# Kernel optimization log

Hardware: AMD Instinct MI355X
Metric: run time of the kernel (lower is better)

Reference implementation:

```python
import jax, jax.numpy as jnp
import numpy as np

EPS = 1e-5


def setup_inputs() -> dict:
    key = jax.random.key(0)
    ks = jax.random.split(key, 4)
    N, E, D, L = 100000, 1600000, 128, 3
    x = jax.random.normal(ks[0], (N, D), dtype=jnp.float32)
    edge_index = jax.random.randint(ks[1], (2, E), 0, N, dtype=jnp.int64)
    # torch Linear weight layout [out, in]; kaiming-ish scale
    W = jax.random.normal(ks[2], (L, D, D), dtype=jnp.float32) / np.sqrt(D)
    b = jnp.zeros((L, D), dtype=jnp.float32)
    gamma = jnp.ones((L, D), dtype=jnp.float32)
    beta = jnp.zeros((L, D), dtype=jnp.float32)
    return {"x": x, "edge_index": edge_index, "W": W, "b": b,
            "gamma": gamma, "beta": beta}


def reference(x, edge_index, W, b, gamma, beta):
    N = x.shape[0]
    L = W.shape[0]
    # add_self_loops
    loops = jnp.arange(N, dtype=edge_index.dtype)
    ei = jnp.concatenate([edge_index, jnp.stack([loops, loops])], axis=1)
    row, col = ei[0], ei[1]  # source, target (PyG source_to_target flow)
    # degree of target nodes (includes self loops)
    deg = jax.ops.segment_sum(jnp.ones(col.shape, x.dtype), col, num_segments=N)
    deg_inv_sqrt = jnp.where(deg > 0, deg ** -0.5, jnp.array(0.0, x.dtype))
    norm = deg_inv_sqrt[row] * deg_inv_sqrt[col]  # [E+N]
    for l in range(L):
        h = x @ W[l].T  # Linear, no bias
        # gather source messages, scale, scatter-add to targets
        out = jax.ops.segment_sum(norm[:, None] * h[row], col, num_segments=N)
        out = out + b[l]
        # NodeNorm 'm': subtract per-node (row) mean over features
        out = out - jnp.mean(out, axis=1, keepdims=True)
        # BatchNorm1d (training mode: biased batch stats over node axis)
        mu = jnp.mean(out, axis=0)
        var = jnp.var(out, axis=0)
        x = gamma[l] * (out - mu) * jax.lax.rsqrt(var + EPS) + beta[l]
    return x
```

## Files before the change

kernel.cpp:

```cpp
#include <hip/hip_runtime.h>

#define D 128
#define EPSV 1e-5f

typedef _Float16 f16;
typedef __attribute__((ext_vector_type(8))) _Float16 f16x8;
typedef __attribute__((ext_vector_type(4))) _Float16 f16x4;
typedef __attribute__((ext_vector_type(4))) float f32x4;

__global__ void fold_kernel(const float* __restrict__ W, const float* __restrict__ stats,
                            const float* __restrict__ gamma, const float* __restrict__ beta,
                            float Ninv, int use_id,
                            f16* __restrict__ Wfo, float* __restrict__ shW) {
    const int o = blockIdx.x;
    const int k = threadIdx.x;
    float w = W[o * D + k];
    float sc = 1.0f, sh = 0.0f;
    if (!use_id) {
        float mu = stats[k] * Ninv;
        float var = stats[D + k] * Ninv - mu * mu;
        float inv = rsqrtf(var + EPSV);
        sc = gamma[k] * inv;
        sh = beta[k] - mu * sc;
    }
    Wfo[o * D + k] = (f16)(w * sc);
    float v = sh * w;
    #pragma unroll
    for (int off = 1; off < 64; off <<= 1) v += __shfl_xor(v, off, 64);
    __shared__ float red[2];
    if ((k & 63) == 0) red[k >> 6] = v;
    __syncthreads();
    if (k == 0) shW[o] = red[0] + red[1];
}

__global__ __launch_bounds__(256) void bcount_kernel(const int* __restrict__ col,
                                                     int* __restrict__ gb, int E, int seg) {
    __shared__ int s[4096];
    for (int j = threadIdx.x; j < seg; j += 256) s[j] = 0;
    __syncthreads();
    int i = blockIdx.x * 256 + threadIdx.x;
    const int stride = gridDim.x * 256;
    for (; i < E; i += stride) {
        int b = col[i] >> 8;
        int p = (i >> 8) & 7;
        atomicAdd(&s[b * 8 + p], 1);
    }
    __syncthreads();
    for (int j = threadIdx.x; j < seg; j += 256)
        if (s[j]) atomicAdd(&gb[j], s[j]);
}

__global__ __launch_bounds__(1024) void bscan_kernel(const int* __restrict__ gb,
                                                     int* __restrict__ soff,
                                                     int* __restrict__ cur) {
    __shared__ int s[1024];
    const int tid = threadIdx.x;
    const int base = tid * 4;
    int g0 = gb[base], g1 = gb[base + 1], g2 = gb[base + 2], g3 = gb[base + 3];
    int my = g0 + g1 + g2 + g3;
    s[tid] = my;
    __syncthreads();
    for (int off = 1; off < 1024; off <<= 1) {
        int t = (tid >= off) ? s[tid - off] : 0;
        __syncthreads();
        s[tid] += t;
        __syncthreads();
    }
    int ex = s[tid] - my;
    soff[base] = ex;           cur[(base + 0) * 16] = ex;  ex += g0;
    soff[base + 1] = ex;       cur[(base + 1) * 16] = ex;  ex += g1;
    soff[base + 2] = ex;       cur[(base + 2) * 16] = ex;  ex += g2;
    soff[base + 3] = ex;       cur[(base + 3) * 16] = ex;
    if (tid == 1023) soff[4096] = s[1023];
}

__global__ __launch_bounds__(256) void bfill_kernel(const int* __restrict__ row,
                                                    const int* __restrict__ col,
                                                    int* __restrict__ cur,
                                                    int* __restrict__ bpairs, int E) {
    int i = blockIdx.x * 256 + threadIdx.x;
    const int stride = gridDim.x * 256;
    for (; i < E; i += stride) {
        int c = col[i];
        int b = c >> 8;
        int p = (i >> 8) & 7;
        int pos = atomicAdd(&cur[(b * 8 + p) * 16], 1);
        bpairs[pos] = (int)(((unsigned)(c & 255) << 24) | (unsigned)row[i]);
    }
}

__global__ __launch_bounds__(256) void bdeg_kernel(const int* __restrict__ bpairs,
                                                   const int* __restrict__ soff,
                                                   int* __restrict__ deg,
                                                   float* __restrict__ dis, int N) {
    __shared__ int dc[256];
    const int b = blockIdx.x;
    const int tid = threadIdx.x;
    dc[tid] = 0;
    __syncthreads();
    const int s0 = soff[b * 8], s1 = soff[(b + 1) * 8];
    for (int k = s0 + tid; k < s1; k += 256)
        atomicAdd(&dc[(unsigned)bpairs[k] >> 24], 1);
    __syncthreads();
    int c = (b << 8) + tid;
    if (c < N) {
        int dv = dc[tid];
        deg[c] = dv;
        dis[c] = rsqrtf((float)dv + 1.0f);
    }
}

__global__ void scan1_kernel(const int* __restrict__ cnt, int* __restrict__ offs,
                             int* __restrict__ bsum, int N) {
    __shared__ int s[256];
    int tid = threadIdx.x;
    int i = blockIdx.x * 256 + tid;
    int v = (i < N) ? cnt[i] : 0;
    s[tid] = v;
    __syncthreads();
    for (int off = 1; off < 256; off <<= 1) {
        int t = (tid >= off) ? s[tid - off] : 0;
        __syncthreads();
        s[tid] += t;
        __syncthreads();
    }
    if (i < N) offs[i] = s[tid] - v;
    if (tid == 255) bsum[blockIdx.x] = s[255];
}

__global__ void scan2_kernel(int* __restrict__ bsum, int NB) {
    __shared__ int s[512];
    int tid = threadIdx.x;
    int v = (tid < NB) ? bsum[tid] : 0;
    s[tid] = v;
    __syncthreads();
    for (int off = 1; off < 512; off <<= 1) {
        int t = (tid >= off) ? s[tid - off] : 0;
        __syncthreads();
        s[tid] += t;
        __syncthreads();
    }
    if (tid < NB) bsum[tid] = s[tid] - v;
}

__global__ void scan3_kernel(int* __restrict__ offs, const int* __restrict__ bsum,
                             int N, int E) {
    int i = blockIdx.x * 256 + threadIdx.x;
    if (i < N) offs[i] += bsum[blockIdx.x];
    if (i == 0) offs[N] = E;
}

__global__ __launch_bounds__(256) void cfill_kernel(const int* __restrict__ bpairs,
                                                    const int* __restrict__ soff,
                                                    const int* __restrict__ offs,
                                                    int* __restrict__ srcs, int N) {
    __shared__ int lc[256];
    const int b = blockIdx.x;
    const int tid = threadIdx.x;
    int c = (b << 8) + tid;
    lc[tid] = (c < N) ? offs[c] : 0;
    __syncthreads();
    const int s0 = soff[b * 8], s1 = soff[(b + 1) * 8];
    for (int k = s0 + tid; k < s1; k += 256) {
        int pk = bpairs[k];
        int pos = atomicAdd(&lc[(unsigned)pk >> 24], 1);
        srcs[pos] = pk & 0x00FFFFFF;
    }
}

__global__ __launch_bounds__(256) void tsort_kernel(const int* __restrict__ deg,
                                                    const int* __restrict__ offs,
                                                    const float* __restrict__ dis,
                                                    int4* __restrict__ nodeinfo, int N) {
    __shared__ int hist[256];
    __shared__ int cur[256];
    __shared__ int cur2[256];
    const int tid = threadIdx.x;
    const int i = blockIdx.x * 256 + tid;
    hist[tid] = 0;
    __syncthreads();
    int b = 0, dv = 0;
    if (i < N) {
        dv = deg[i];
        b = 255 - min(dv, 255);
        atomicAdd(&hist[b], 1);
    }
    __syncthreads();
    int v = hist[tid];
    cur[tid] = v;
    __syncthreads();
    for (int off = 1; off < 256; off <<= 1) {
        int t = (tid >= off) ? cur[tid - off] : 0;
        __syncthreads();
        cur[tid] += t;
        __syncthreads();
    }
    cur2[tid] = cur[tid] - v;
    __syncthreads();
    if (i < N) {
        int pos = atomicAdd(&cur2[b], 1);
        nodeinfo[blockIdx.x * 256 + pos] =
            make_int4(i, offs[i], dv, __float_as_int(dis[i]));
    }
}


__global__ __launch_bounds__(256) void gemm_kernel(
    const f16* __restrict__ xh, const float* __restrict__ xf32,
    const f16* __restrict__ Wfo, const float* __restrict__ shW,
    const float* __restrict__ dis, f16* __restrict__ h, int N, int nrg)
{
    const int lane = threadIdx.x & 63;
    const int l15 = lane & 15;
    const int lh = lane >> 4;

    f16x8 af[8][4];
    #pragma unroll
    for (int t = 0; t < 8; t++)
        #pragma unroll
        for (int kb = 0; kb < 4; kb++)
            af[t][kb] = *reinterpret_cast<const f16x8*>(
                &Wfo[(t * 16 + l15) * D + kb * 32 + lh * 8]);

    const int wid = (blockIdx.x * blockDim.x + threadIdx.x) >> 6;
    const int nwaves = (gridDim.x * blockDim.x) >> 6;

    for (int rg = wid; rg < nrg; rg += nwaves) {
        int row = rg * 16 + l15;
        int rrow = min(row, N - 1);
        f16x8 bf[4];
        if (xf32) {
            #pragma unroll
            for (int kb = 0; kb < 4; kb++) {
                const float* p = &xf32[(long long)rrow * D + kb * 32 + lh * 8];
                float4 u0 = *reinterpret_cast<const float4*>(p);
                float4 u1 = *reinterpret_cast<const float4*>(p + 4);
                f16x8 b;
                b[0] = (f16)u0.x; b[1] = (f16)u0.y; b[2] = (f16)u0.z; b[3] = (f16)u0.w;
                b[4] = (f16)u1.x; b[5] = (f16)u1.y; b[6] = (f16)u1.z; b[7] = (f16)u1.w;
                bf[kb] = b;
            }
        } else {
            #pragma unroll
            for (int kb = 0; kb < 4; kb++)
                bf[kb] = *reinterpret_cast<const f16x8*>(
                    &xh[(long long)rrow * D + kb * 32 + lh * 8]);
        }
        float d = dis[rrow];
        bool ok = (row < N);

        #pragma unroll
        for (int t = 0; t < 8; t++) {
            f32x4 acc = {0.0f, 0.0f, 0.0f, 0.0f};
            #pragma unroll
            for (int kb = 0; kb < 4; kb++)
                acc = __builtin_amdgcn_mfma_f32_16x16x32_f16(af[t][kb], bf[kb], acc, 0, 0, 0);
            int o0 = t * 16 + lh * 4;
            float4 sw = *reinterpret_cast<const float4*>(&shW[o0]);
            f16x4 ov;
            ov[0] = (f16)(d * (acc[0] + sw.x));
            ov[1] = (f16)(d * (acc[1] + sw.y));
            ov[2] = (f16)(d * (acc[2] + sw.z));
            ov[3] = (f16)(d * (acc[3] + sw.w));
            if (ok)
                *reinterpret_cast<f16x4*>(&h[(long long)row * D + o0]) = ov;
        }
    }
}

__global__ __launch_bounds__(256) void gather_kernel(
    const f16* __restrict__ h, const int4* __restrict__ nodeinfo,
    const int* __restrict__ srcs, const float* __restrict__ bias,
    f16* __restrict__ t, float* __restrict__ stats, int N, int E)
{
    const int tid = threadIdx.x;
    const int l16 = tid & 15;
    const int grp = tid >> 4;
    const int f8 = l16 * 8;
    float bv[8];
    {
        float4 ba = *reinterpret_cast<const float4*>(&bias[f8]);
        float4 bb = *reinterpret_cast<const float4*>(&bias[f8 + 4]);
        bv[0] = ba.x; bv[1] = ba.y; bv[2] = ba.z; bv[3] = ba.w;
        bv[4] = bb.x; bv[5] = bb.y; bv[6] = bb.z; bv[7] = bb.w;
    }
    float ssum[8] = {0, 0, 0, 0, 0, 0, 0, 0}, ssq[8] = {0, 0, 0, 0, 0, 0, 0, 0};

    const int ci = blockIdx.x * 32 + grp * 2;
    if (ci < N) {
        const bool v1 = (ci + 1 < N);
        const int4 niA = nodeinfo[ci];
        const int4 niB = v1 ? nodeinfo[ci + 1] : niA;

        const int c0 = niA.x, k00 = niA.y, d0 = niA.z;
        const float dis0 = __int_as_float(niA.w);
        const int c1 = niB.x;
        const int k10 = v1 ? niB.y : 0;
        const int d1 = v1 ? niB.z : 0;
        const float dis1 = v1 ? __int_as_float(niB.w) : 0.0f;

        f16x8 s0v = *reinterpret_cast<const f16x8*>(&h[(long long)c0 * D + f8]);
        f16x8 s1v = *reinterpret_cast<const f16x8*>(&h[(long long)c1 * D + f8]);
        float a0[8], a1[8];
        #pragma unroll
        for (int m = 0; m < 8; m++) { a0[m] = (float)s0v[m]; a1[m] = (float)s1v[m]; }

        const int maxd = max(d0, d1);
        for (int kb = 0; kb < maxd; kb += 16) {
            int i0 = min(k00 + kb + l16, E - 1);
            int i1 = min(k10 + kb + l16, E - 1);
            int rl0 = srcs[i0];
            int rl1 = srcs[i1];
            int cnt0 = min(16, d0 - kb);
            int cnt1 = min(16, d1 - kb);
            int cmax = max(cnt0, cnt1);
            for (int j = 0; j < cmax; j += 2) {
                int r00 = __shfl(rl0, j, 16);
                int r01 = __shfl(rl0, j + 1, 16);
                int r10 = __shfl(rl1, j, 16);
                int r11 = __shfl(rl1, j + 1, 16);
                float w00 = (j < cnt0) ? 1.0f : 0.0f;
                float w01 = (j + 1 < cnt0) ? 1.0f : 0.0f;
                float w10 = (j < cnt1) ? 1.0f : 0.0f;
                float w11 = (j + 1 < cnt1) ? 1.0f : 0.0f;
                f16x8 v00 = *reinterpret_cast<const f16x8*>(&h[(long long)r00 * D + f8]);
                f16x8 v01 = *reinterpret_cast<const f16x8*>(&h[(long long)r01 * D + f8]);
                f16x8 v10 = *reinterpret_cast<const f16x8*>(&h[(long long)r10 * D + f8]);
                f16x8 v11 = *reinterpret_cast<const f16x8*>(&h[(long long)r11 * D + f8]);
                #pragma unroll
                for (int m = 0; m < 8; m++) {
                    a0[m] = fmaf(w00, (float)v00[m], a0[m]);
                    a0[m] = fmaf(w01, (float)v01[m], a0[m]);
                    a1[m] = fmaf(w10, (float)v10[m], a1[m]);
                    a1[m] = fmaf(w11, (float)v11[m], a1[m]);
                }
            }
        }

        {
            float tv[8], s = 0.0f;
            #pragma unroll
            for (int m = 0; m < 8; m++) { tv[m] = dis0 * a0[m] + bv[m]; s += tv[m]; }
            #pragma unroll
            for (int off = 1; off < 16; off <<= 1) s += __shfl_xor(s, off, 16);
            float mean = s * (1.0f / 128.0f);
            f16x8 ov;
            #pragma unroll
            for (int m = 0; m < 8; m++) {
                tv[m] -= mean;
                ov[m] = (f16)tv[m];
                ssum[m] += tv[m];
                ssq[m] += tv[m] * tv[m];
            }
            *reinterpret_cast<f16x8*>(&t[(long long)c0 * D + f8]) = ov;
        }
        {
            float g = v1 ? 1.0f : 0.0f;
            float tv[8], s = 0.0f;
            #pragma unroll
            for (int m = 0; m < 8; m++) { tv[m] = dis1 * a1[m] + bv[m]; s += tv[m]; }
            #pragma unroll
            for (int off = 1; off < 16; off <<= 1) s += __shfl_xor(s, off, 16);
            float mean = s * (1.0f / 128.0f);
            f16x8 ov;
            #pragma unroll
            for (int m = 0; m < 8; m++) {
                tv[m] -= mean;
                ov[m] = (f16)tv[m];
                ssum[m] += g * tv[m];
                ssq[m] += g * tv[m] * tv[m];
            }
            if (v1)
                *reinterpret_cast<f16x8*>(&t[(long long)c1 * D + f8]) = ov;
        }
    }

    __shared__ float red[256 * 16];
    #pragma unroll
    for (int j = 0; j < 8; j++) {
        red[tid * 16 + j] = ssum[j];
        red[tid * 16 + 8 + j] = ssq[j];
    }
    __syncthreads();
    const int o = tid;
    const int f = o & 127;
    const int sq = o >> 7;
    const int lf = f >> 3;
    const int j = f & 7;
    float v = 0;
    #pragma unroll
    for (int g = 0; g < 16; g++)
        v += red[(g * 16 + lf) * 16 + sq * 8 + j];
    unsafeAtomicAdd(&stats[o], v);
}

__global__ __launch_bounds__(256) void epi2_kernel(
    const f16* __restrict__ t, const float* __restrict__ stats,
    const float* __restrict__ gamma, const float* __restrict__ beta,
    float Ninv, float* __restrict__ out, long long total4)
{
    __shared__ float sc[D], sh[D];
    if (threadIdx.x < D) {
        int j = threadIdx.x;
        float mu = stats[j] * Ninv;
        float var = stats[D + j] * Ninv - mu * mu;
        float inv = rsqrtf(var + EPSV);
        float s = gamma[j] * inv;
        sc[j] = s;
        sh[j] = beta[j] - mu * s;
    }
    __syncthreads();
    long long i = (long long)blockIdx.x * blockDim.x + threadIdx.x;
    const long long stride = (long long)gridDim.x * blockDim.x;
    for (; i < total4; i += stride) {
        f16x4 v = reinterpret_cast<const f16x4*>(t)[i];
        int f0 = (int)((i * 4) & (D - 1));
        float4 o;
        o.x = (float)v[0] * sc[f0 + 0] + sh[f0 + 0];
        o.y = (float)v[1] * sc[f0 + 1] + sh[f0 + 1];
        o.z = (float)v[2] * sc[f0 + 2] + sh[f0 + 2];
        o.w = (float)v[3] * sc[f0 + 3] + sh[f0 + 3];
        reinterpret_cast<float4*>(out)[i] = o;
    }
}

extern "C" void kernel_launch(void* const* d_in, const int* in_sizes, int n_in,
                              void* d_out, int out_size, void* d_ws, size_t ws_size,
                              hipStream_t stream)
{
    const float* x_in  = (const float*)d_in[0];
    const int*   ei    = (const int*)d_in[1];
    const float* W     = (const float*)d_in[2];
    const float* bias  = (const float*)d_in[3];
    const float* gamma = (const float*)d_in[4];
    const float* beta  = (const float*)d_in[5];

    const int N = in_sizes[0] / D;
    const int E = in_sizes[1] / 2;
    const int L = in_sizes[2] / (D * D);
    const int* row = ei;
    const int* col = ei + E;
    const int NB = (N + 255) / 256;
    const int NBUCK = (N + 255) >> 8;
    const int seg = NBUCK * 8;
    const int nrg = (N + 15) / 16;

    f16* tbuf = (f16*)d_ws;
    f16* hbuf = tbuf + (size_t)N * D;
    f16* Wfo  = hbuf + (size_t)N * D;
    float* dis   = (float*)(Wfo + D * D);
    float* stats = dis + N;
    float* shW   = stats + 2 * D;
    size_t offf = (size_t)(shW + D - (float*)d_ws);
    offf = (offf + 3) & ~(size_t)3;
    int4* nodeinfo = (int4*)((float*)d_ws + offf);
    int* deg    = (int*)(nodeinfo + (size_t)NB * 256);
    int* offs   = deg + N;
    int* srcs   = offs + (N + 1);
    int* bsum   = srcs + (E + 16);
    int* gb     = bsum + 512;
    int* soff   = gb + 4096;
    int* cur    = soff + 4097;
    int* bpairs = cur + 4096 * 16;

    hipMemsetAsync(gb, 0, 4096 * sizeof(int), stream);
    bcount_kernel<<<128, 256, 0, stream>>>(col, gb, E, seg);
    bscan_kernel<<<1, 1024, 0, stream>>>(gb, soff, cur);
    bfill_kernel<<<1024, 256, 0, stream>>>(row, col, cur, bpairs, E);
    bdeg_kernel<<<NBUCK, 256, 0, stream>>>(bpairs, soff, deg, dis, N);
    scan1_kernel<<<NB, 256, 0, stream>>>(deg, offs, bsum, N);
    scan2_kernel<<<1, 512, 0, stream>>>(bsum, NB);
    scan3_kernel<<<NB, 256, 0, stream>>>(offs, bsum, N, E);
    cfill_kernel<<<NBUCK, 256, 0, stream>>>(bpairs, soff, offs, srcs, N);
    tsort_kernel<<<NB, 256, 0, stream>>>(deg, offs, dis, nodeinfo, N);

    const float Ninv = 1.0f / (float)N;
    const long long total4 = (long long)N * D / 4;
    const int gblocks = (N + 31) / 32;

    fold_kernel<<<D, D, 0, stream>>>(W, stats, gamma, beta, Ninv, 1, Wfo, shW);

    for (int l = 0; l < L; l++) {
        gemm_kernel<<<512, 256, 0, stream>>>(
            tbuf, (l == 0) ? x_in : nullptr, Wfo, shW, dis, hbuf, N, nrg);
        hipMemsetAsync(stats, 0, 2 * D * sizeof(float), stream);
        gather_kernel<<<gblocks, 256, 0, stream>>>(
            hbuf, nodeinfo, srcs, bias + (size_t)l * D, tbuf, stats, N, E);
        if (l < L - 1)
            fold_kernel<<<D, D, 0, stream>>>(
                W + (size_t)(l + 1) * D * D, stats, gamma + (size_t)(l + 1) * D,
                beta + (size_t)(l + 1) * D, Ninv, 0, Wfo, shW);
        else
            epi2_kernel<<<4096, 256, 0, stream>>>(
                tbuf, stats, gamma + (size_t)l * D, beta + (size_t)l * D,
                Ninv, (float*)d_out, total4);
    }
}
```

Measured before the change: 536.8 us.

## Fuse CSR build kernels into one and loop gather with nodeinfo prefetch

```diff
diff --git a/kernel.cpp b/kernel.cpp
--- a/kernel.cpp
+++ b/kernel.cpp
@@ -89,11 +89,14 @@
     }
 }
 
-__global__ __launch_bounds__(256) void bdeg_kernel(const int* __restrict__ bpairs,
-                                                   const int* __restrict__ soff,
-                                                   int* __restrict__ deg,
-                                                   float* __restrict__ dis, int N) {
+__global__ __launch_bounds__(256) void build_kernel(
+    const int* __restrict__ bpairs, const int* __restrict__ soff,
+    float* __restrict__ dis, int4* __restrict__ nodeinfo,
+    int* __restrict__ srcs, int N)
+{
     __shared__ int dc[256];
+    __shared__ int pf[256];
+    __shared__ int cur2[256];
     const int b = blockIdx.x;
     const int tid = threadIdx.x;
     dc[tid] = 0;
@@ -102,105 +105,50 @@
     for (int k = s0 + tid; k < s1; k += 256)
         atomicAdd(&dc[(unsigned)bpairs[k] >> 24], 1);
     __syncthreads();
-    int c = (b << 8) + tid;
+    const int dv = dc[tid];
+    pf[tid] = dv;
+    __syncthreads();
+    for (int off = 1; off < 256; off <<= 1) {
+        int t = (tid >= off) ? pf[tid - off] : 0;
+        __syncthreads();
+        pf[tid] += t;
+        __syncthreads();
+    }
+    const int myoff = s0 + pf[tid] - dv;
+    const int c = (b << 8) + tid;
+    const float disv = rsqrtf((float)dv + 1.0f);
+    if (c < N) dis[c] = disv;
+    __syncthreads();
+    pf[tid] = 0;
+    __syncthreads();
+    int bin = 0;
     if (c < N) {
-        int dv = dc[tid];
-        deg[c] = dv;
-        dis[c] = rsqrtf((float)dv + 1.0f);
-    }
-}
-
-__global__ void scan1_kernel(const int* __restrict__ cnt, int* __restrict__ offs,
-                             int* __restrict__ bsum, int N) {
-    __shared__ int s[256];
-    int tid = threadIdx.x;
-    int i = blockIdx.x * 256 + tid;
-    int v = (i < N) ? cnt[i] : 0;
-    s[tid] = v;
+        bin = 255 - min(dv, 255);
+        atomicAdd(&pf[bin], 1);
+    }
+    __syncthreads();
+    int hv = pf[tid];
+    cur2[tid] = hv;
     __syncthreads();
     for (int off = 1; off < 256; off <<= 1) {
-        int t = (tid >= off) ? s[tid - off] : 0;
-        __syncthreads();
-        s[tid] += t;
-        __syncthreads();
-    }
-    if (i < N) offs[i] = s[tid] - v;
-    if (tid == 255) bsum[blockIdx.x] = s[255];
-}
-
-__global__ void scan2_kernel(int* __restrict__ bsum, int NB) {
-    __shared__ int s[512];
-    int tid = threadIdx.x;
-    int v = (tid < NB) ? bsum[tid] : 0;
-    s[tid] = v;
-    __syncthreads();
-    for (int off = 1; off < 512; off <<= 1) {
-        int t = (tid >= off) ? s[tid - off] : 0;
-        __syncthreads();
-        s[tid] += t;
-        __syncthreads();
-    }
-    if (tid < NB) bsum[tid] = s[tid] - v;
-}
-
-__global__ void scan3_kernel(int* __restrict__ offs, const int* __restrict__ bsum,
-                             int N, int E) {
-    int i = blockIdx.x * 256 + threadIdx.x;
-    if (i < N) offs[i] += bsum[blockIdx.x];
-    if (i == 0) offs[N] = E;
-}
-
-__global__ __launch_bounds__(256) void cfill_kernel(const int* __restrict__ bpairs,
-                                                    const int* __restrict__ soff,
-                                                    const int* __restrict__ offs,
-                                                    int* __restrict__ srcs, int N) {
-    __shared__ int lc[256];
-    const int b = blockIdx.x;
-    const int tid = threadIdx.x;
-    int c = (b << 8) + tid;
-    lc[tid] = (c < N) ? offs[c] : 0;
-    __syncthreads();
-    const int s0 = soff[b * 8], s1 = soff[(b + 1) * 8];
+        int t = (tid >= off) ? cur2[tid - off] : 0;
+        __syncthreads();
+        cur2[tid] += t;
+        __syncthreads();
+    }
+    cur2[tid] -= hv;
+    __syncthreads();
+    if (c < N) {
+        int pos = atomicAdd(&cur2[bin], 1);
+        nodeinfo[b * 256 + pos] = make_int4(c, myoff, dv, __float_as_int(disv));
+    }
+    __syncthreads();
+    dc[tid] = myoff;
+    __syncthreads();
     for (int k = s0 + tid; k < s1; k += 256) {
         int pk = bpairs[k];
-        int pos = atomicAdd(&lc[(unsigned)pk >> 24], 1);
+        int pos = atomicAdd(&dc[(unsigned)pk >> 24], 1);
         srcs[pos] = pk & 0x00FFFFFF;
-    }
-}
-
-__global__ __launch_bounds__(256) void tsort_kernel(const int* __restrict__ deg,
-                                                    const int* __restrict__ offs,
-                                                    const float* __restrict__ dis,
-                                                    int4* __restrict__ nodeinfo, int N) {
-    __shared__ int hist[256];
-    __shared__ int cur[256];
-    __shared__ int cur2[256];
-    const int tid = threadIdx.x;
-    const int i = blockIdx.x * 256 + tid;
-    hist[tid] = 0;
-    __syncthreads();
-    int b = 0, dv = 0;
-    if (i < N) {
-        dv = deg[i];
-        b = 255 - min(dv, 255);
-        atomicAdd(&hist[b], 1);
-    }
-    __syncthreads();
-    int v = hist[tid];
-    cur[tid] = v;
-    __syncthreads();
-    for (int off = 1; off < 256; off <<= 1) {
-        int t = (tid >= off) ? cur[tid - off] : 0;
-        __syncthreads();
-        cur[tid] += t;
-        __syncthreads();
-    }
-    cur2[tid] = cur[tid] - v;
-    __syncthreads();
-    if (i < N) {
-        int pos = atomicAdd(&cur2[b], 1);
-        nodeinfo[blockIdx.x * 256 + pos] =
-            make_int4(i, offs[i], dv, __float_as_int(dis[i]));
     }
 }
 
@@ -208,8 +156,11 @@
 __global__ __launch_bounds__(256) void gemm_kernel(
     const f16* __restrict__ xh, const float* __restrict__ xf32,
     const f16* __restrict__ Wfo, const float* __restrict__ shW,
-    const float* __restrict__ dis, f16* __restrict__ h, int N, int nrg)
+    const float* __restrict__ dis, f16* __restrict__ h,
+    float* __restrict__ stats, int N, int nrg)
 {
+    if (blockIdx.x == 0) stats[threadIdx.x] = 0.0f;
+
     const int lane = threadIdx.x & 63;
     const int l15 = lane & 15;
     const int lh = lane >> 4;
@@ -268,7 +219,7 @@
     }
 }
 
-__global__ __launch_bounds__(256) void gather_kernel(
+__global__ __launch_bounds__(128) void gather_kernel(
     const f16* __restrict__ h, const int4* __restrict__ nodeinfo,
     const int* __restrict__ srcs, const float* __restrict__ bias,
     f16* __restrict__ t, float* __restrict__ stats, int N, int E)
@@ -286,15 +237,21 @@
     }
     float ssum[8] = {0, 0, 0, 0, 0, 0, 0, 0}, ssq[8] = {0, 0, 0, 0, 0, 0, 0, 0};
 
-    const int ci = blockIdx.x * 32 + grp * 2;
-    if (ci < N) {
+    int ci = blockIdx.x * 16 + grp * 2;
+    const int cstride = gridDim.x * 16;
+    const int4 zero4 = make_int4(0, 0, 0, 0);
+    int4 niA = (ci < N) ? nodeinfo[ci] : zero4;
+    int4 niB = (ci + 1 < N) ? nodeinfo[ci + 1] : zero4;
+
+    for (; ci < N; ci += cstride) {
+        const int cin = ci + cstride;
+        int4 niA_n = (cin < N) ? nodeinfo[cin] : zero4;
+        int4 niB_n = (cin + 1 < N) ? nodeinfo[cin + 1] : zero4;
+
         const bool v1 = (ci + 1 < N);
-        const int4 niA = nodeinfo[ci];
-        const int4 niB = v1 ? nodeinfo[ci + 1] : niA;
-
         const int c0 = niA.x, k00 = niA.y, d0 = niA.z;
         const float dis0 = __int_as_float(niA.w);
-        const int c1 = niB.x;
+        const int c1 = v1 ? niB.x : c0;
         const int k10 = v1 ? niB.y : 0;
         const int d1 = v1 ? niB.z : 0;
         const float dis1 = v1 ? __int_as_float(niB.w) : 0.0f;
@@ -373,25 +330,30 @@
             if (v1)
                 *reinterpret_cast<f16x8*>(&t[(long long)c1 * D + f8]) = ov;
         }
-    }
-
-    __shared__ float red[256 * 16];
+        niA = niA_n;
+        niB = niB_n;
+    }
+
+    __shared__ float red[128 * 16];
     #pragma unroll
     for (int j = 0; j < 8; j++) {
         red[tid * 16 + j] = ssum[j];
         red[tid * 16 + 8 + j] = ssq[j];
     }
     __syncthreads();
-    const int o = tid;
-    const int f = o & 127;
-    const int sq = o >> 7;
-    const int lf = f >> 3;
-    const int j = f & 7;
-    float v = 0;
     #pragma unroll
-    for (int g = 0; g < 16; g++)
-        v += red[(g * 16 + lf) * 16 + sq * 8 + j];
-    unsafeAtomicAdd(&stats[o], v);
+    for (int oo = 0; oo < 2; oo++) {
+        const int o = tid + oo * 128;
+        const int f = o & 127;
+        const int sq = o >> 7;
+        const int lf = f >> 3;
+        const int j = f & 7;
+        float v = 0;
+        #pragma unroll
+        for (int g = 0; g < 8; g++)
+            v += red[(g * 16 + lf) * 16 + sq * 8 + j];
+        unsafeAtomicAdd(&stats[o], v);
+    }
 }
 
 __global__ __launch_bounds__(256) void epi2_kernel(
@@ -454,11 +416,8 @@
     size_t offf = (size_t)(shW + D - (float*)d_ws);
     offf = (offf + 3) & ~(size_t)3;
     int4* nodeinfo = (int4*)((float*)d_ws + offf);
-    int* deg    = (int*)(nodeinfo + (size_t)NB * 256);
-    int* offs   = deg + N;
-    int* srcs   = offs + (N + 1);
-    int* bsum   = srcs + (E + 16);
-    int* gb     = bsum + 512;
+    int* srcs   = (int*)(nodeinfo + (size_t)NB * 256);
+    int* gb     = srcs + (E + 16);
     int* soff   = gb + 4096;
     int* cur    = soff + 4097;
     int* bpairs = cur + 4096 * 16;
@@ -467,12 +426,7 @@
     bcount_kernel<<<128, 256, 0, stream>>>(col, gb, E, seg);
     bscan_kernel<<<1, 1024, 0, stream>>>(gb, soff, cur);
     bfill_kernel<<<1024, 256, 0, stream>>>(row, col, cur, bpairs, E);
-    bdeg_kernel<<<NBUCK, 256, 0, stream>>>(bpairs, soff, deg, dis, N);
-    scan1_kernel<<<NB, 256, 0, stream>>>(deg, offs, bsum, N);
-    scan2_kernel<<<1, 512, 0, stream>>>(bsum, NB);
-    scan3_kernel<<<NB, 256, 0, stream>>>(offs, bsum, N, E);
-    cfill_kernel<<<NBUCK, 256, 0, stream>>>(bpairs, soff, offs, srcs, N);
-    tsort_kernel<<<NB, 256, 0, stream>>>(deg, offs, dis, nodeinfo, N);
+    build_kernel<<<NBUCK, 256, 0, stream>>>(bpairs, soff, dis, nodeinfo, srcs, N);
 
     const float Ninv = 1.0f / (float)N;
     const long long total4 = (long long)N * D / 4;
@@ -482,9 +436,8 @@
 
     for (int l = 0; l < L; l++) {
         gemm_kernel<<<512, 256, 0, stream>>>(
-            tbuf, (l == 0) ? x_in : nullptr, Wfo, shW, dis, hbuf, N, nrg);
-        hipMemsetAsync(stats, 0, 2 * D * sizeof(float), stream);
-        gather_kernel<<<gblocks, 256, 0, stream>>>(
+            tbuf, (l == 0) ? x_in : nullptr, Wfo, shW, dis, hbuf, stats, N, nrg);
+        gather_kernel<<<gblocks, 128, 0, stream>>>(
             hbuf, nodeinfo, srcs, bias + (size_t)l * D, tbuf, stats, N, E);
         if (l < L - 1)
             fold_kernel<<<D, D, 0, stream>>>(
```

New measurement: 560.8 us. 1.04x slower.
